# Optimization experiments

Hardware: AMD Instinct MI355X
Metric: run time of the kernel (lower is better)

## Reference

```python
import jax, jax.numpy as jnp
import numpy as np

N, NNODES, CIN, COUT = 64, 512, 32, 64


def setup_inputs() -> dict:
    key = jax.random.key(0)
    k1, k2, k3, k4, k5 = jax.random.split(key, 5)
    A = jax.random.normal(k1, (N, NNODES, NNODES), dtype=jnp.float32)
    X = jax.random.normal(k2, (N, NNODES, CIN), dtype=jnp.float32)
    A_coeffs = jax.random.normal(k3, (5 + 2 * CIN,), dtype=jnp.float32)
    x_num = 4 + 2 * CIN
    scale = np.sqrt(2.0) / (COUT + x_num)
    X_coeffs_1 = jax.random.normal(k4, (COUT, x_num), dtype=jnp.float32) * scale
    X_coeffs_2 = jax.random.normal(k5, (COUT, x_num), dtype=jnp.float32) * scale
    return {"A": A, "X": X, "A_coeffs": A_coeffs,
            "X_coeffs_1": X_coeffs_1, "X_coeffs_2": X_coeffs_2}


def _forward(A, X, A_coeffs, W1, W2):
    n = A.shape[-1]
    C = X.shape[-1]
    Xt = jnp.swapaxes(X, -1, -2)                      # N,C,n
    diag = jnp.diagonal(A, axis1=-2, axis2=-1)        # N,n
    mean_diag = diag.mean(-1)                         # N
    mean_cols = A.mean(-1)                            # N,n
    mean_all = mean_cols.mean(-1)                     # N
    mean_X = Xt.mean(-1)                              # N,C

    c = A_coeffs
    w6 = c[5:5 + C]                                   # coeffs for a6 (X_i + X_j)
    w7 = c[5 + C:5 + 2 * C]                           # coeffs for a7 (mean_X)
    # Fold the 'd,ndij->nij' contraction over the 7 basis tensors into
    # scalar/row/col broadcast terms (identical math, no N x (5+2C) x n x n tensor).
    s = jnp.einsum('c,nci->ni', w6, Xt)               # N,n
    const = c[1] * mean_all + c[2] * mean_diag + jnp.einsum('c,nc->n', w7, mean_X)
    vec = c[3] * mean_cols + c[4] * diag + s          # N,n
    A_t = c[0] * A + const[:, None, None] + vec[:, :, None] + vec[:, None, :]

    # X basis out_x: N x (4+2C) x n, order [x1, x2, x3, x4, x5, x6]
    ones_n = jnp.ones((1, 1, n), A.dtype)
    out_x = jnp.concatenate([
        Xt,                                           # x1: N,C,n
        mean_X[:, :, None] * ones_n,                  # x2: N,C,n
        mean_cols[:, None, :],                        # x3: N,1,n
        diag[:, None, :],                             # x4: N,1,n
        mean_diag[:, None, None] * ones_n,            # x5: N,1,n
        mean_all[:, None, None] * ones_n,             # x6: N,1,n
    ], axis=1)
    X1 = jnp.einsum('bd,ndi->nbi', W1, out_x)         # N,B,n
    X2 = jnp.einsum('bd,ndi->nbi', W2, out_x)         # N,B,n
    out = jnp.einsum('nij,nbj->nbi', A_t, X1) / n + X2  # N,B,n
    return jnp.swapaxes(out, -1, -2)                  # N,n,B


def reference(A, X, A_coeffs, X_coeffs_1, X_coeffs_2):
    return _forward(A, X, A_coeffs, X_coeffs_1, X_coeffs_2)
```

## Files before the change

### kernel.cpp

```cpp
#include <hip/hip_runtime.h>
#include <hip/hip_bf16.h>

#define NB 64
#define NN 512
#define CI 32
#define CO 64
#define XN 68

typedef __attribute__((ext_vector_type(8))) short bf16x8;
typedef __attribute__((ext_vector_type(4))) float f32x4;

__device__ inline short f2bf(float f) {
  union { __hip_bfloat16 h; unsigned short u; } cv;
  cv.h = __float2bfloat16(f);
  return (short)cv.u;
}

__device__ inline bf16x8 cvt8(float4 a, float4 b) {
  bf16x8 r;
  r[0] = f2bf(a.x); r[1] = f2bf(a.y); r[2] = f2bf(a.z); r[3] = f2bf(a.w);
  r[4] = f2bf(b.x); r[5] = f2bf(b.y); r[6] = f2bf(b.z); r[7] = f2bf(b.w);
  return r;
}

__global__ __launch_bounds__(256) void k1x(
    const float* __restrict__ A, const float* __restrict__ X,
    const float* __restrict__ cf, const float* __restrict__ W1,
    float* __restrict__ mc, float* __restrict__ dg, float* __restrict__ vec,
    float* __restrict__ pA, float* __restrict__ pD,
    float* __restrict__ pmX, float* __restrict__ ptC, float* __restrict__ pS,
    unsigned short* __restrict__ Ybf) {
  int b = blockIdx.x, ch = blockIdx.y;
  int t = threadIdx.x, w = t >> 6, lane = t & 63;
  int r0 = ch * 16;
  int kb = r0 >> 5, jbase = r0 & 16;
  const float* Ab = A + (size_t)b * NN * NN;
  __shared__ float sXc[16][33];
  __shared__ float scf[69];
  __shared__ float sMc[16], sDg[16], sVec[16], wsum[4];

  if (t < 69) scf[t] = cf[t];
  {
    int j = t >> 4, c = (t & 15) * 2;
    float2 xv = *(const float2*)(X + ((size_t)b * NN + r0 + j) * CI + c);
    sXc[j][c] = xv.x; sXc[j][c + 1] = xv.y;
  }
  float4 v0[4], v1[4];
#pragma unroll
  for (int m = 0; m < 4; ++m) {
    const float* rp = Ab + (size_t)(r0 + w * 4 + m) * NN;
    v0[m] = *(const float4*)(rp + lane * 4);
    v1[m] = *(const float4*)(rp + 256 + lane * 4);
  }
  float accR = 0.f;
#pragma unroll
  for (int m = 0; m < 4; ++m) {
    float s = (v0[m].x + v0[m].y) + (v0[m].z + v0[m].w) +
              (v1[m].x + v1[m].y) + (v1[m].z + v1[m].w);
#pragma unroll
    for (int off = 1; off < 64; off <<= 1) s += __shfl_xor(s, off, 64);
    if (lane == 0) {
      float m_ = s * (1.0f / NN);
      mc[b * NN + r0 + w * 4 + m] = m_;
      sMc[w * 4 + m] = m_;
    }
    accR += s;
  }
  if (lane == 0) wsum[w] = accR;
  if (t < 16) {
    float d = Ab[(size_t)(r0 + t) * NN + r0 + t];
    dg[b * NN + r0 + t] = d;
    sDg[t] = d;
  }
  __syncthreads();

  float c0n = scf[0] * (1.0f / NN);

  if (t < 16) {
    float u = 0.f;
#pragma unroll
    for (int c = 0; c < CI; ++c) u += scf[5 + c] * sXc[t][c];
    float vj = scf[3] * sMc[t] + scf[4] * sDg[t] + u;
    vec[b * NN + r0 + t] = vj;
    sVec[t] = vj;
  } else if (t == 16) {
    pA[b * 32 + ch] = wsum[0] + wsum[1] + wsum[2] + wsum[3];
    float sd = 0.f;
#pragma unroll
    for (int k = 0; k < 16; ++k) sd += sDg[k];
    pD[b * 32 + ch] = sd;
  }

  {
    int ra = lane & 15, kg = lane >> 4, g = lane >> 4;
    const float* wp = W1 + (w * 16 + ra) * XN + kg * 8;
    bf16x8 wf = cvt8(*(const float4*)wp, *(const float4*)(wp + 4));
    const float* xp = &sXc[ra][kg * 8];
    bf16x8 xf = cvt8(*(const float4*)xp, *(const float4*)(xp + 4));
    f32x4 zero = {0.f, 0.f, 0.f, 0.f};
    f32x4 d = __builtin_amdgcn_mfma_f32_16x16x32_bf16(xf, wf, zero, 0, 0, 0);
    union { unsigned short u[4]; uint2 v; } pk;
#pragma unroll
    for (int r = 0; r < 4; ++r) pk.u[r] = (unsigned short)f2bf(d[r] * c0n);
    int o = w * 16 + ra;
    *(uint2*)(Ybf + (((size_t)b * 16 + kb) * 80 + o) * 32 + jbase + g * 4) = pk.v;
  }
  if (t < 16) {
    Ybf[(((size_t)b * 16 + kb) * 80 + 64) * 32 + jbase + t] =
        (unsigned short)f2bf(sMc[t] * c0n);
  } else if (t < 32) {
    Ybf[(((size_t)b * 16 + kb) * 80 + 65) * 32 + jbase + (t - 16)] =
        (unsigned short)f2bf(sDg[t - 16] * c0n);
  } else if (t < 32 + 224) {
    int u2 = t - 32;
    int row = 66 + (u2 >> 4), col = jbase + (u2 & 15);
    Ybf[(((size_t)b * 16 + kb) * 80 + row) * 32 + col] = 0;
  }
  __syncthreads();

  if (t < 32) {
    float s1 = 0.f, s2 = 0.f;
#pragma unroll
    for (int r = 0; r < 16; ++r) {
      float xv = sXc[r][t];
      s1 += xv;
      s2 += sVec[r] * xv;
    }
    pmX[((size_t)b * 32 + ch) * 32 + t] = s1;
    ptC[((size_t)b * 32 + ch) * 32 + t] = s2;
  } else if (t < 35) {
    float s = 0.f;
    if (t == 32) { for (int r = 0; r < 16; ++r) s += sVec[r]; }
    if (t == 33) { for (int r = 0; r < 16; ++r) s += sVec[r] * sMc[r]; }
    if (t == 34) { for (int r = 0; r < 16; ++r) s += sVec[r] * sDg[r]; }
    pS[((size_t)b * 32 + ch) * 3 + (t - 32)] = s;
  }
}

__global__ __launch_bounds__(256) void kW(
    const float* __restrict__ cf, const float* __restrict__ W1,
    const float* __restrict__ W2, const float* __restrict__ pA,
    const float* __restrict__ pD, const float* __restrict__ pmX,
    const float* __restrict__ ptC, const float* __restrict__ pS,
    float* __restrict__ colv, float* __restrict__ sconst) {
  int gb = blockIdx.x, t = threadIdx.x;
  int bb0 = gb * 4;
  __shared__ float sW1[64][69], sW2[64][69];
  __shared__ float mXs[4][33], tCs[4][33];
  __shared__ float scal[4][6];
  __shared__ float scf[69];
  if (t < 69) scf[t] = cf[t];
  for (int idx = t; idx < 64 * XN; idx += 256) {
    int r = idx / XN, c = idx - r * XN;
    sW1[r][c] = W1[idx];
    sW2[r][c] = W2[idx];
  }
  if (t < 128) {
    int bb = t >> 5, c = t & 31, b = bb0 + bb;
    float s1 = 0.f, s2 = 0.f;
#pragma unroll
    for (int k = 0; k < 32; ++k) {
      s1 += pmX[((size_t)b * 32 + k) * 32 + c];
      s2 += ptC[((size_t)b * 32 + k) * 32 + c];
    }
    mXs[bb][c] = s1 * (1.0f / NN);
    tCs[bb][c] = s2;
  } else if (t < 132) {
    int bb = t - 128, b = bb0 + bb;
    float sA = 0.f, sD = 0.f;
#pragma unroll
    for (int k = 0; k < 32; ++k) { sA += pA[b * 32 + k]; sD += pD[b * 32 + k]; }
    scal[bb][0] = sD * (1.0f / NN);
    scal[bb][1] = sA * (1.0f / ((float)NN * (float)NN));
  } else if (t < 136) {
    int bb = t - 132, b = bb0 + bb;
    float s1 = 0.f, s2 = 0.f, s3 = 0.f;
#pragma unroll
    for (int k = 0; k < 32; ++k) {
      s1 += pS[((size_t)b * 32 + k) * 3 + 0];
      s2 += pS[((size_t)b * 32 + k) * 3 + 1];
      s3 += pS[((size_t)b * 32 + k) * 3 + 2];
    }
    scal[bb][2] = s1; scal[bb][3] = s2; scal[bb][4] = s3;
  }
  __syncthreads();
  if (t < 4) {
    float s7 = 0.f;
#pragma unroll
    for (int c = 0; c < CI; ++c) s7 += scf[5 + CI + c] * mXs[t][c];
    sconst[bb0 + t] = scf[1] * scal[t][1] + scf[2] * scal[t][0] + s7;
  }
  {
    int bb = t >> 6, o = t & 63, b = bb0 + bb;
    float w1mX = 0.f, a1 = 0.f, a2 = 0.f, wt = 0.f;
#pragma unroll
    for (int c = 0; c < CI; ++c) {
      float m = mXs[bb][c];
      w1mX += sW1[o][c] * m;
      a1 += sW1[o][CI + c] * m;
      a2 += sW2[o][CI + c] * m;
      wt += sW1[o][c] * tCs[bb][c];
    }
    float smd = scal[bb][0], sma = scal[bb][1];
    a1 += sW1[o][66] * smd + sW1[o][67] * sma;
    a2 += sW2[o][66] * smd + sW2[o][67] * sma;
    float we0 = sW1[o][64], we1 = sW1[o][65];
    float S1n = w1mX + a1 + we0 * sma + we1 * smd;
    float SVn = (wt + a1 * scal[bb][2] + we0 * scal[bb][3] + we1 * scal[bb][4]) * (1.0f / NN);
    float4 cva = make_float4(S1n, a2 + SVn, sW2[o][64] + scf[0] * a1, sW2[o][65]);
    float4 cvb = make_float4(we0, we1, 0.f, 0.f);
    *(float4*)&colv[((size_t)b * CO + o) * 8] = cva;
    *(float4*)&colv[((size_t)b * CO + o) * 8 + 4] = cvb;
  }
}

__global__ __launch_bounds__(256, 4) void k5_mfma(
    const float* __restrict__ A, const unsigned short* __restrict__ Ybf,
    const float* __restrict__ X, const float* __restrict__ W2,
    const float* __restrict__ vec, const float* __restrict__ mc,
    const float* __restrict__ dg, const float* __restrict__ colv,
    const float* __restrict__ sconst, float* __restrict__ out) {
  int ic = blockIdx.x, b = blockIdx.y;
  int t = threadIdx.x, w = t >> 6, lane = t & 63;
  int rg = w >> 1, oc = w & 1;
  int ra = lane & 15, kg = lane >> 4, g = lane >> 4;
  int i0 = ic * 32;
  int wr0 = rg * 16;
  __shared__ unsigned short sA[2][32 * 64];
  __shared__ float sGm[32], sGd[32];

  const unsigned short* Yb = Ybf + (size_t)b * 16 * 80 * 32;

  int st_r = t >> 3, st_k = t & 7;
  const float* Agl = A + ((size_t)(b * NN + i0 + st_r)) * NN + st_k * 8;
  int st_addr = st_r * 64 + ((st_k ^ (st_r & 7)) << 3);

  {
    float4 a0 = *(const float4*)(Agl);
    float4 a1 = *(const float4*)(Agl + 4);
    *(bf16x8*)&sA[0][st_addr] = cvt8(a0, a1);
  }
  __syncthreads();

  f32x4 acc[2] = {{0.f, 0.f, 0.f, 0.f}, {0.f, 0.f, 0.f, 0.f}};
  f32x4 acc4 = {0.f, 0.f, 0.f, 0.f};
  int arow = wr0 + ra;
  int abase = arow * 64;
  int aswz = arow & 7;

  for (int c = 0; c < 8; ++c) {
    int cur = c & 1;
    float4 na0, na1;
    if (c < 7) {
      na0 = *(const float4*)(Agl + (c + 1) * 64);
      na1 = *(const float4*)(Agl + (c + 1) * 64 + 4);
    }
#pragma unroll
    for (int kbl = 0; kbl < 2; ++kbl) {
      int kb = c * 2 + kbl;
      bf16x8 af = *(const bf16x8*)&sA[cur][abase + (((kbl * 4 + kg) ^ aswz) << 3)];
      const unsigned short* Ybb = Yb + ((size_t)kb * 80) * 32;
#pragma unroll
      for (int to = 0; to < 2; ++to) {
        bf16x8 bf = *(const bf16x8*)(Ybb + (oc * 32 + to * 16 + ra) * 32 + kg * 8);
        acc[to] = __builtin_amdgcn_mfma_f32_16x16x32_bf16(af, bf, acc[to], 0, 0, 0);
      }
      if (oc == 0) {
        bf16x8 bf4 = *(const bf16x8*)(Ybb + (64 + ra) * 32 + kg * 8);
        acc4 = __builtin_amdgcn_mfma_f32_16x16x32_bf16(af, bf4, acc4, 0, 0, 0);
      }
    }
    if (c < 7) {
      *(bf16x8*)&sA[cur ^ 1][st_addr] = cvt8(na0, na1);
    }
    __syncthreads();
  }

  {
    const float* xp = X + (size_t)(b * NN + i0 + wr0 + ra) * CI + kg * 8;
    bf16x8 xf = cvt8(*(const float4*)xp, *(const float4*)(xp + 4));
#pragma unroll
    for (int to = 0; to < 2; ++to) {
      const float* wp = W2 + (size_t)(oc * 32 + to * 16 + ra) * XN + kg * 8;
      bf16x8 wf = cvt8(*(const float4*)wp, *(const float4*)(wp + 4));
      acc[to] = __builtin_amdgcn_mfma_f32_16x16x32_bf16(xf, wf, acc[to], 0, 0, 0);
    }
  }

  if (oc == 0 && ra < 2) {
#pragma unroll
    for (int r = 0; r < 4; ++r) {
      if (ra == 0) sGm[wr0 + g * 4 + r] = acc4[r];
      else         sGd[wr0 + g * 4 + r] = acc4[r];
    }
  }
  __syncthreads();

  float4 v4 = *(const float4*)&vec[b * NN + i0 + wr0 + g * 4];
  float4 m4 = *(const float4*)&mc[b * NN + i0 + wr0 + g * 4];
  float4 d4 = *(const float4*)&dg[b * NN + i0 + wr0 + g * 4];
  float sc = sconst[b];
  float vp[4] = {v4.x + sc, v4.y + sc, v4.z + sc, v4.w + sc};
  float mr[4] = {m4.x, m4.y, m4.z, m4.w};
  float dr[4] = {d4.x, d4.y, d4.z, d4.w};
  float Gm[4], Gd[4];
#pragma unroll
  for (int r = 0; r < 4; ++r) {
    int row = wr0 + g * 4 + r;
    Gm[r] = sGm[row];
    Gd[r] = sGd[row];
  }

#pragma unroll
  for (int to = 0; to < 2; ++to) {
    int o = oc * 32 + to * 16 + ra;
    float4 cva = *(const float4*)&colv[((size_t)b * CO + o) * 8];
    float4 cvb = *(const float4*)&colv[((size_t)b * CO + o) * 8 + 4];
#pragma unroll
    for (int r = 0; r < 4; ++r) {
      float val = acc[to][r] + vp[r] * cva.x + cva.y + mr[r] * cva.z +
                  dr[r] * cva.w + Gm[r] * cvb.x + Gd[r] * cvb.y;
      out[((size_t)(b * NN + i0 + wr0 + g * 4 + r)) * CO + o] = val;
    }
  }
}

extern "C" void kernel_launch(void* const* d_in, const int* in_sizes, int n_in,
                              void* d_out, int out_size, void* d_ws, size_t ws_size,
                              hipStream_t stream) {
  const float* A = (const float*)d_in[0];
  const float* X = (const float*)d_in[1];
  const float* cf = (const float*)d_in[2];
  const float* W1 = (const float*)d_in[3];
  const float* W2 = (const float*)d_in[4];
  float* out = (float*)d_out;

  float* p = (float*)d_ws;
  float* mc = p;      p += NB * NN;
  float* dg = p;      p += NB * NN;
  float* vec = p;     p += NB * NN;
  float* pA = p;      p += NB * 32;
  float* pD = p;      p += NB * 32;
  float* pmX = p;     p += NB * 32 * 32;
  float* ptC = p;     p += NB * 32 * 32;
  float* pS = p;      p += NB * 32 * 3;
  float* colv = p;    p += NB * CO * 8;
  float* sconst = p;  p += NB;
  unsigned short* Ybf = (unsigned short*)p;

  k1x<<<dim3(NB, 32), 256, 0, stream>>>(A, X, cf, W1, mc, dg, vec,
                                        pA, pD, pmX, ptC, pS, Ybf);
  kW<<<16, 256, 0, stream>>>(cf, W1, W2, pA, pD, pmX, ptC, pS, colv, sconst);
  k5_mfma<<<dim3(16, NB), 256, 0, stream>>>(A, Ybf, X, W2, vec, mc, dg,
                                            colv, sconst, out);
}
```

Measured before the change: 49.54 us.

## Pre-convert A to swizzled bf16 in first pass and stream tiles via global_load_lds

The first kernel, which already reads A for row means, now also writes a bf16 copy of A in a pre-swizzled tile layout. The MFMA kernel reads that copy instead of fp32 A. It stages both the A and Y tiles into LDS with direct global-to-LDS loads, and uses 512-thread blocks covering 64 rows. This halves A traffic in the second pass and removes per-thread conversion and register staging. The cost is an extra bf16 write of A (half its fp32 size) in k1x, more LDS per block, and possible breakage if the parts of the epilogue not shown still assume 32-row tiles.

```diff
diff --git a/kernel.cpp b/kernel.cpp
--- a/kernel.cpp
+++ b/kernel.cpp
@@ -21,6 +21,12 @@
   r[0] = f2bf(a.x); r[1] = f2bf(a.y); r[2] = f2bf(a.z); r[3] = f2bf(a.w);
   r[4] = f2bf(b.x); r[5] = f2bf(b.y); r[6] = f2bf(b.z); r[7] = f2bf(b.w);
   return r;
+}
+
+__device__ __forceinline__ void gld16(const void* g, void* l) {
+  __builtin_amdgcn_global_load_lds(
+      (const __attribute__((address_space(1))) unsigned int*)g,
+      (__attribute__((address_space(3))) unsigned int*)l, 16, 0, 0);
 }
 
 __global__ __launch_bounds__(256) void k1x(
@@ -29,7 +35,7 @@
     float* __restrict__ mc, float* __restrict__ dg, float* __restrict__ vec,
     float* __restrict__ pA, float* __restrict__ pD,
     float* __restrict__ pmX, float* __restrict__ ptC, float* __restrict__ pS,
-    unsigned short* __restrict__ Ybf) {
+    unsigned short* __restrict__ Ybf, unsigned short* __restrict__ Abf) {
   int b = blockIdx.x, ch = blockIdx.y;
   int t = threadIdx.x, w = t >> 6, lane = t & 63;
   int r0 = ch * 16;
@@ -71,6 +77,27 @@
     float d = Ab[(size_t)(r0 + t) * NN + r0 + t];
     dg[b * NN + r0 + t] = d;
     sDg[t] = d;
+  }
+
+  {
+    int ic5 = ch >> 2;
+    int lrb = (ch & 3) * 16 + w * 4;
+    size_t bb = ((size_t)(b * 8 + ic5)) * 8 * 4096;
+    int c5a = lane >> 4;
+    int Ka = (lane & 15) >> 1;
+    int sub = (lane & 1) << 2;
+#pragma unroll
+    for (int m = 0; m < 4; ++m) {
+      int lr = lrb + m;
+      int sl = ((Ka ^ (lr & 7)) << 3) + sub;
+      union { unsigned short u[4]; uint2 v; } p0, p1;
+      p0.u[0] = (unsigned short)f2bf(v0[m].x); p0.u[1] = (unsigned short)f2bf(v0[m].y);
+      p0.u[2] = (unsigned short)f2bf(v0[m].z); p0.u[3] = (unsigned short)f2bf(v0[m].w);
+      p1.u[0] = (unsigned short)f2bf(v1[m].x); p1.u[1] = (unsigned short)f2bf(v1[m].y);
+      p1.u[2] = (unsigned short)f2bf(v1[m].z); p1.u[3] = (unsigned short)f2bf(v1[m].w);
+      *(uint2*)(Abf + bb + (size_t)c5a * 4096 + lr * 64 + sl) = p0.v;
+      *(uint2*)(Abf + bb + (size_t)(4 + c5a) * 4096 + lr * 64 + sl) = p1.v;
+    }
   }
   __syncthreads();
 
@@ -214,8 +241,8 @@
   }
 }
 
-__global__ __launch_bounds__(256, 4) void k5_mfma(
-    const float* __restrict__ A, const unsigned short* __restrict__ Ybf,
+__global__ __launch_bounds__(512, 8) void k5_mfma(
+    const unsigned short* __restrict__ Abf, const unsigned short* __restrict__ Ybf,
     const float* __restrict__ X, const float* __restrict__ W2,
     const float* __restrict__ vec, const float* __restrict__ mc,
     const float* __restrict__ dg, const float* __restrict__ colv,
@@ -224,21 +251,22 @@
   int t = threadIdx.x, w = t >> 6, lane = t & 63;
   int rg = w >> 1, oc = w & 1;
   int ra = lane & 15, kg = lane >> 4, g = lane >> 4;
-  int i0 = ic * 32;
+  int i0 = ic * 64;
   int wr0 = rg * 16;
-  __shared__ unsigned short sA[2][32 * 64];
-  __shared__ float sGm[32], sGd[32];
-
-  const unsigned short* Yb = Ybf + (size_t)b * 16 * 80 * 32;
-
-  int st_r = t >> 3, st_k = t & 7;
-  const float* Agl = A + ((size_t)(b * NN + i0 + st_r)) * NN + st_k * 8;
-  int st_addr = st_r * 64 + ((st_k ^ (st_r & 7)) << 3);
-
-  {
-    float4 a0 = *(const float4*)(Agl);
-    float4 a1 = *(const float4*)(Agl + 4);
-    *(bf16x8*)&sA[0][st_addr] = cvt8(a0, a1);
+  __shared__ unsigned short sA[2][4096];
+  __shared__ unsigned short sB[2][5120];
+  __shared__ float sGm[64], sGd[64];
+
+  const unsigned short* Asrc = Abf + ((size_t)(b * 8 + ic)) * 8 * 4096;
+  const unsigned short* Bsrc = Ybf + (size_t)b * 16 * 80 * 32;
+
+  int aoff = w * 512 + lane * 8;
+  int boff2 = (8 + w) * 512 + lane * 8;
+
+  {
+    gld16(Asrc + aoff, &sA[0][w * 512]);
+    gld16(Bsrc + aoff, &sB[0][w * 512]);
+    if (w < 2) gld16(Bsrc + boff2, &sB[0][(8 + w) * 512]);
   }
   __syncthreads();
 
@@ -250,28 +278,26 @@
 
   for (int c = 0; c < 8; ++c) {
     int cur = c & 1;
-    float4 na0, na1;
     if (c < 7) {
-      na0 = *(const float4*)(Agl + (c + 1) * 64);
-      na1 = *(const float4*)(Agl + (c + 1) * 64 + 4);
+      const unsigned short* an = Asrc + (size_t)(c + 1) * 4096;
+      const unsigned short* bn = Bsrc + (size_t)(c + 1) * 5120;
+      gld16(an + aoff, &sA[cur ^ 1][w * 512]);
+      gld16(bn + aoff, &sB[cur ^ 1][w * 512]);
+      if (w < 2) gld16(bn + boff2, &sB[cur ^ 1][(8 + w) * 512]);
     }
 #pragma unroll
     for (int kbl = 0; kbl < 2; ++kbl) {
-      int kb = c * 2 + kbl;
       bf16x8 af = *(const bf16x8*)&sA[cur][abase + (((kbl * 4 + kg) ^ aswz) << 3)];
-      const unsigned short* Ybb = Yb + ((size_t)kb * 80) * 32;
 #pragma unroll
       for (int to = 0; to < 2; ++to) {
-        bf16x8 bf = *(const bf16x8*)(Ybb + (oc * 32 + to * 16 + ra) * 32 + kg * 8);
+        int grow = kbl * 80 + oc * 32 + to * 16 + ra;
+        bf16x8 bf = *(const bf16x8*)&sB[cur][grow * 32 + kg * 8];
         acc[to] = __builtin_amdgcn_mfma_f32_16x16x32_bf16(af, bf, acc[to], 0, 0, 0);
       }
       if (oc == 0) {
-        bf16x8 bf4 = *(const bf16x8*)(Ybb + (64 + ra) * 32 + kg * 8);
+        bf16x8 bf4 = *(const bf16x8*)&sB[cur][(kbl * 80 + 64 + ra) * 32 + kg * 8];
         acc4 = __builtin_amdgcn_mfma_f32_16x16x32_bf16(af, bf4, acc4, 0, 0, 0);
       }
-    }
-    if (c < 7) {
-      *(bf16x8*)&sA[cur ^ 1][st_addr] = cvt8(na0, na1);
     }
     __syncthreads();
   }
@@ -347,10 +373,11 @@
   float* colv = p;    p += NB * CO * 8;
   float* sconst = p;  p += NB;
   unsigned short* Ybf = (unsigned short*)p;
+  unsigned short* Abf = Ybf + (size_t)NB * 16 * 80 * 32;
 
   k1x<<<dim3(NB, 32), 256, 0, stream>>>(A, X, cf, W1, mc, dg, vec,
-                                        pA, pD, pmX, ptC, pS, Ybf);
+                                        pA, pD, pmX, ptC, pS, Ybf, Abf);
   kW<<<16, 256, 0, stream>>>(cf, W1, W2, pA, pD, pmX, ptC, pS, colv, sconst);
-  k5_mfma<<<dim3(16, NB), 256, 0, stream>>>(A, Ybf, X, W2, vec, mc, dg,
-                                            colv, sconst, out);
-}
+  k5_mfma<<<dim3(8, NB), 512, 0, stream>>>(Abf, Ybf, X, W2, vec, mc, dg,
+                                           colv, sconst, out);
+}
```

New measurement: 45.99 us. 1.08x faster.
